# Kernel optimization log

Hardware: AMD Instinct MI355X
Metric: run time of the kernel (lower is better)

The kernel has to match this reference:

```python
import jax, jax.numpy as jnp
import numpy as np

EMBED_DIM = 768
NUM_HEADS = 12
HEAD_DIM = EMBED_DIM // NUM_HEADS
SCALE = HEAD_DIM ** -0.5


def setup_inputs() -> dict:
    key = jax.random.key(0)
    k_x, k_qkv, k_pw, k_pb = jax.random.split(key, 4)
    B, N = 2, 4096
    x = jax.random.normal(k_x, (B, N, EMBED_DIM), dtype=jnp.float32)
    # nn.Linear weights stored as [out, in]; we keep [in, out] for x @ W
    w_qkv = jax.random.normal(k_qkv, (EMBED_DIM, 3 * EMBED_DIM), dtype=jnp.float32) * (EMBED_DIM ** -0.5)
    w_proj = jax.random.normal(k_pw, (EMBED_DIM, EMBED_DIM), dtype=jnp.float32) * (EMBED_DIM ** -0.5)
    b_proj = jax.random.normal(k_pb, (EMBED_DIM,), dtype=jnp.float32) * 0.02
    return {"x": x, "w_qkv": w_qkv, "w_proj": w_proj, "b_proj": b_proj}


def reference(x, w_qkv, w_proj, b_proj):
    B, N, D = x.shape
    H, hd = NUM_HEADS, HEAD_DIM
    qkv = x @ w_qkv                                   # [B, N, 3*D]
    qkv = qkv.reshape(B, N, 3, H, hd)                 # matches '(qkv h d)' split order
    q, k, v = (qkv[:, :, i].transpose(0, 2, 1, 3) for i in range(3))  # each [B, H, N, hd]
    attn = jnp.einsum('bhid,bhjd->bhij', q, k) * SCALE  # [B, H, N, N] fully materialized
    attn = jax.nn.softmax(attn, axis=-1)
    out = jnp.einsum('bhij,bhjd->bhid', attn, v)        # [B, H, N, hd]
    out = out.transpose(0, 2, 1, 3).reshape(B, N, D)    # 'b h n d -> b n (h d)'
    return out @ w_proj + b_proj
```

## Files before the change

### kernel.cpp

```cpp
#include <hip/hip_runtime.h>
#include <hip/hip_bf16.h>

typedef __attribute__((ext_vector_type(4))) float f32x4;
typedef __attribute__((ext_vector_type(4))) int i32x4;
typedef __attribute__((ext_vector_type(8))) short s16x8;

static constexpr int NB = 2, NH = 12, SEQ = 4096, DM = 768, HD = 64;
static constexpr int ROWS = NB * SEQ;
static constexpr float QSC = 0.125f * 1.44269504f;

#define MFMA(a, b, c) __builtin_amdgcn_mfma_f32_16x16x32_bf16((a), (b), (c), 0, 0, 0)

typedef const void __attribute__((address_space(1)))* gas_t;
typedef void __attribute__((address_space(3)))* las_t;

__device__ __forceinline__ short f2bf(float f) {
  union { float f; unsigned u; } v; v.f = f;
  unsigned r = v.u + 0x7fffu + ((v.u >> 16) & 1u);
  return (short)(r >> 16);
}

__device__ __forceinline__ float exp2v(float x) {
  float r; asm("v_exp_f32 %0, %1" : "=v"(r) : "v"(x)); return r;
}

__global__ __launch_bounds__(256) void k_cast4(const float* __restrict__ in,
                                               short* __restrict__ out, int n4) {
  int i = blockIdx.x * 256 + threadIdx.x;
  if (i < n4) {
    float4 v = reinterpret_cast<const float4*>(in)[i];
    short4 o = { f2bf(v.x), f2bf(v.y), f2bf(v.z), f2bf(v.w) };
    reinterpret_cast<short4*>(out)[i] = o;
  }
}

__global__ __launch_bounds__(256) void k_tcast2(const float* __restrict__ in,
                                                short* __restrict__ out, int r, int c) {
  __shared__ short tile[32][33];
  int tpc = c >> 5;
  int by = blockIdx.x / tpc, bx = blockIdx.x % tpc;
  int tx = threadIdx.x & 31, ty = threadIdx.x >> 5;
#pragma unroll
  for (int i = 0; i < 4; ++i)
    tile[ty + i * 8][tx] = f2bf(in[(size_t)(by * 32 + ty + i * 8) * c + bx * 32 + tx]);
  __syncthreads();
#pragma unroll
  for (int i = 0; i < 4; ++i)
    out[(size_t)(bx * 32 + ty + i * 8) * r + by * 32 + tx] = tile[tx][ty + i * 8];
}

__device__ __forceinline__ void gemm128(const short* __restrict__ A,
                                        const short* __restrict__ Bt,
                                        int K, int row0, int col0,
                                        short As[2][4096], short Bs[2][4096],
                                        f32x4 acc[4][4]) {
  int w = threadIdx.x >> 6, l = threadIdx.x & 63;
  int q = l & 15, g = l >> 4;
  int wr = w >> 1, wc = w & 1;
  int sr = w * 16 + (l >> 2);
  int sc = (l & 3) * 8;

#define STG(buf, k0)                                                           \
  {                                                                            \
    _Pragma("unroll")                                                          \
    for (int i = 0; i < 2; ++i) {                                              \
      __builtin_amdgcn_global_load_lds(                                        \
          (gas_t)(A + (size_t)(row0 + i * 64 + sr) * K + (k0) + sc),           \
          (las_t)&As[buf][i * 2048 + w * 512], 16, 0, 0);                      \
      __builtin_amdgcn_global_load_lds(                                        \
          (gas_t)(Bt + (size_t)(col0 + i * 64 + sr) * K + (k0) + sc),          \
          (las_t)&Bs[buf][i * 2048 + w * 512], 16, 0, 0);                      \
    }                                                                          \
  }

  STG(0, 0);
  __syncthreads();
  int cur = 0;
  for (int k0 = 0; k0 < K; k0 += 32) {
    if (k0 + 32 < K) STG(cur ^ 1, k0 + 32);
    s16x8 af[4], bf[4];
#pragma unroll
    for (int m = 0; m < 4; ++m)
      af[m] = *reinterpret_cast<const s16x8*>(&As[cur][(wr * 64 + m * 16 + q) * 32 + g * 8]);
#pragma unroll
    for (int n = 0; n < 4; ++n)
      bf[n] = *reinterpret_cast<const s16x8*>(&Bs[cur][(wc * 64 + n * 16 + q) * 32 + g * 8]);
#pragma unroll
    for (int m = 0; m < 4; ++m)
#pragma unroll
      for (int n = 0; n < 4; ++n)
        acc[m][n] = MFMA(af[m], bf[n], acc[m][n]);
    __syncthreads();
    cur ^= 1;
  }
#undef STG
}

__global__ __launch_bounds__(256) void k_gemm_qkv2(const short* __restrict__ xb,
                                                   const short* __restrict__ wt,
                                                   short* __restrict__ qw,
                                                   short* __restrict__ kw,
                                                   short* __restrict__ vtw) {
  __shared__ __align__(16) short As[2][4096], Bs[2][4096];
  int bid = blockIdx.x;
  int swz = (bid & 7) * 144 + (bid >> 3);
  int brow = swz / 18, bcol = swz % 18;
  int row0 = brow * 128, col0 = bcol * 128;
  f32x4 acc[4][4] = {};
  gemm128(xb, wt, DM, row0, col0, As, Bs, acc);

  int w = threadIdx.x >> 6, l = threadIdx.x & 63;
  int q = l & 15, g = l >> 4;
  int wr = w >> 1, wc = w & 1;
  int cb = col0 + wc * 64;
  int which = cb / DM, h = (cb % DM) >> 6;
  int rowb = row0 + wr * 64;
  int b = rowb >> 12;
  int bh = b * NH + h;
#pragma unroll
  for (int m = 0; m < 4; ++m) {
#pragma unroll
    for (int n = 0; n < 4; ++n) {
      int d = n * 16 + q;
      if (which == 2) {
        int nseq = (rowb & 4095) + m * 16 + g * 4;
        short4 ov = { f2bf(acc[m][n][0]), f2bf(acc[m][n][1]),
                      f2bf(acc[m][n][2]), f2bf(acc[m][n][3]) };
        *reinterpret_cast<short4*>(&vtw[((size_t)bh * HD + d) * SEQ + nseq]) = ov;
      } else {
        short* dst = (which == 0) ? qw : kw;
        float sc = (which == 0) ? QSC : 1.f;
#pragma unroll
        for (int r = 0; r < 4; ++r) {
          int nseq = (rowb & 4095) + m * 16 + g * 4 + r;
          dst[((size_t)bh * SEQ + nseq) * HD + d] = f2bf(acc[m][n][r] * sc);
        }
      }
    }
  }
}

__global__ __launch_bounds__(256) void k_gemm_proj2(const short* __restrict__ aob,
                                                    const short* __restrict__ wt,
                                                    const float* __restrict__ bias,
                                                    float* __restrict__ out) {
  __shared__ __align__(16) short As[2][4096], Bs[2][4096];
  int bid = blockIdx.x;
  int swz = (bid & 7) * 48 + (bid >> 3);
  int brow = swz / 6, bcol = swz % 6;
  int row0 = brow * 128, col0 = bcol * 128;
  f32x4 acc[4][4] = {};
  gemm128(aob, wt, DM, row0, col0, As, Bs, acc);

  int w = threadIdx.x >> 6, l = threadIdx.x & 63;
  int q = l & 15, g = l >> 4;
  int wr = w >> 1, wc = w & 1;
#pragma unroll
  for (int m = 0; m < 4; ++m)
#pragma unroll
    for (int n = 0; n < 4; ++n) {
      int col = col0 + wc * 64 + n * 16 + q;
      float bv = bias[col];
#pragma unroll
      for (int r = 0; r < 4; ++r) {
        int row = row0 + wr * 64 + m * 16 + g * 4 + r;
        out[(size_t)row * DM + col] = acc[m][n][r] + bv;
      }
    }
}

__global__ __launch_bounds__(256, 2) void k_attn13(const short* __restrict__ qw,
                                                   const short* __restrict__ kw,
                                                   const short* __restrict__ vtw,
                                                   short* __restrict__ ao) {
  __shared__ __align__(16) short lds[2][2][4096];

  int bid = blockIdx.x;
  int swz = (bid & 7) * 48 + (bid >> 3);
  int bh = swz >> 4;
  int qchunk = swz & 15;

  int w = threadIdx.x >> 6, l = threadIdx.x & 63;
  int q = l & 15, g = l >> 4;

  const short* Kg = kw + (size_t)bh * SEQ * HD;
  const short* Vg = vtw + (size_t)bh * HD * SEQ;

  int ss = (l & 7) ^ (l >> 3) ^ ((w & 1) << 2);
  int rst = w * 8 + (l >> 3);

  int qbase = qchunk * 256 + w * 64;
  s16x8 qf[4][2];
#pragma unroll
  for (int qt = 0; qt < 4; ++qt)
#pragma unroll
    for (int kh = 0; kh < 2; ++kh)
      qf[qt][kh] = *reinterpret_cast<const s16x8*>(
          qw + ((size_t)bh * SEQ + qbase + qt * 16 + q) * HD + kh * 32 + g * 8);

  s16x8 ones;
  {
    short o1 = (q == 0) ? (short)0x3F80 : (short)0;
#pragma unroll
    for (int i = 0; i < 8; ++i) ones[i] = o1;
  }

  f32x4 o[4][4] = {};
  f32x4 lsa[4] = {};

#define STAGE(buf, t)                                                              \
  {                                                                                \
    int key0 = (t) * 64;                                                           \
    _Pragma("unroll")                                                              \
    for (int i = 0; i < 2; ++i) {                                                  \
      const short* gk = Kg + (size_t)(key0 + i * 32 + rst) * HD + ss * 8;          \
      __builtin_amdgcn_global_load_lds((gas_t)gk,                                  \
          (las_t)&lds[buf][0][i * 2048 + w * 512], 16, 0, 0);                      \
      const short* gv = Vg + (size_t)(i * 32 + rst) * SEQ + key0 + ss * 8;         \
      __builtin_amdgcn_global_load_lds((gas_t)gv,                                  \
          (las_t)&lds[buf][1][i * 2048 + w * 512], 16, 0, 0);                      \
    }                                                                              \
  }

#define TBODY(CUR, NXT, tt, DO_STAGE)                                              \
  {                                                                                \
    if (DO_STAGE) STAGE(NXT, (tt) + 1);                                            \
    f32x4 s[2][2][4] = {};                              \
    __builtin_amdgcn_s_setprio(1);                                                 \
    _Pragma("unroll")                                                              \
    for (int c = 0; c < 2; ++c)                                                    \
      _Pragma("unroll")                                                            \
      for (int ab = 0; ab < 2; ++ab) {                                             \
        int R = c * 32 + ab * 4 + ((q >> 2) << 3) + (q & 3);                       \
        int sw = (R & 7) ^ (((R >> 3) & 1) << 2);                                  \
        _Pragma("unroll")                                                          \
        for (int kh = 0; kh < 2; ++kh) {                                           \
          int slot = (kh * 4 + g) ^ sw;                                            \
          s16x8 af = *reinterpret_cast<const s16x8*>(                              \
              &lds[CUR][0][R * 64 + slot * 8]);                                    \
          _Pragma("unroll")                                                        \
          for (int qt = 0; qt < 4; ++qt)                                           \
            s[c][ab][qt] = MFMA(af, qf[qt][kh], s[c][ab][qt]);                     \
        }                                                                          \
      }                                                                            \
    __builtin_amdgcn_s_setprio(0);                                                 \
    i32x4 pv[2][4];                                    \
    _Pragma("unroll")                                                              \
    for (int qt = 0; qt < 4; ++qt) {                                               \
      unsigned u[16];                                                              \
      _Pragma("unroll")                                                            \
      for (int i = 0; i < 16; ++i)                                                 \
        u[i] = __float_as_uint(exp2v(s[i >> 3][(i >> 2) & 1][qt][i & 3]));         \
      _Pragma("unroll")                                                            \
      for (int c = 0; c < 2; ++c)                                                  \
        _Pragma("unroll")                                                          \
        for (int j = 0; j < 4; ++j)                                                \
          pv[c][qt][j] = (int)__builtin_amdgcn_perm(u[c * 8 + 2 * j + 1],          \
                                                    u[c * 8 + 2 * j],              \
                                                    0x07060302u);                  \
    }                                                                              \
    __builtin_amdgcn_s_setprio(1);                                                 \
    _Pragma("unroll")                                                              \
    for (int c = 0; c < 2; ++c) {                                                  \
      _Pragma("unroll")                                                            \
      for (int dt = 0; dt < 4; ++dt) {                                             \
        int R = dt * 16 + q;                                                       \
        int sw = (R & 7) ^ (((R >> 3) & 1) << 2);                                  \
        int slot = (c * 4 + g) ^ sw;                                               \
        s16x8 vf = *reinterpret_cast<const s16x8*>(                                \
            &lds[CUR][1][R * 64 + slot * 8]);                                      \
        _Pragma("unroll")                                                          \
        for (int qt = 0; qt < 4; ++qt)                                             \
          o[qt][dt] = MFMA(vf, __builtin_bit_cast(s16x8, pv[c][qt]), o[qt][dt]);   \
      }                                                                            \
      _Pragma("unroll")                                                            \
      for (int qt = 0; qt < 4; ++qt)                                               \
        lsa[qt] = MFMA(ones, __builtin_bit_cast(s16x8, pv[c][qt]), lsa[qt]);       \
    }                                                                              \
    __builtin_amdgcn_s_setprio(0);                                                 \
    __syncthreads();                                                               \
  }

  STAGE(0, 0);
  __syncthreads();

  for (int t = 0; t < SEQ / 64 - 2; t += 2) {
    TBODY(0, 1, t, true);
    TBODY(1, 0, t + 1, true);
  }
  TBODY(0, 1, SEQ / 64 - 2, true);
  TBODY(1, 0, SEQ / 64 - 1, false);
#undef TBODY
#undef STAGE

  int b = bh / NH, h = bh % NH;
#pragma unroll
  for (int qt = 0; qt < 4; ++qt) {
    float ls = __shfl(lsa[qt][0], q);
    float inv = 1.f / ls;
    size_t row = (size_t)b * SEQ + qbase + qt * 16 + q;
    short* op = ao + row * DM + h * HD;
#pragma unroll
    for (int dt = 0; dt < 4; ++dt) {
      short4 ov = { f2bf(o[qt][dt][0] * inv), f2bf(o[qt][dt][1] * inv),
                    f2bf(o[qt][dt][2] * inv), f2bf(o[qt][dt][3] * inv) };
      *reinterpret_cast<short4*>(op + dt * 16 + g * 4) = ov;
    }
  }
}

extern "C" void kernel_launch(void* const* d_in, const int* in_sizes, int n_in,
                              void* d_out, int out_size, void* d_ws, size_t ws_size,
                              hipStream_t stream) {
  const float* x      = (const float*)d_in[0];
  const float* w_qkv  = (const float*)d_in[1];
  const float* w_proj = (const float*)d_in[2];
  const float* b_proj = (const float*)d_in[3];
  float* out = (float*)d_out;

  char* p = (char*)d_ws;
  auto take = [&](size_t bytes) { char* r = p; p += (bytes + 255) & ~(size_t)255; return r; };
  short* xb     = (short*)take((size_t)ROWS * DM * 2);
  short* wtqkv  = (short*)take((size_t)3 * DM * DM * 2);
  short* wtproj = (short*)take((size_t)DM * DM * 2);
  short* qw     = (short*)take((size_t)NB * NH * SEQ * HD * 2);
  short* kw     = (short*)take((size_t)NB * NH * SEQ * HD * 2);
  short* vtw    = (short*)take((size_t)NB * NH * HD * SEQ * 2);
  short* ao     = (short*)take((size_t)ROWS * DM * 2);

  int n4 = ROWS * DM / 4;
  k_cast4<<<(n4 + 255) / 256, 256, 0, stream>>>(x, xb, n4);
  k_tcast2<<<(DM / 32) * (3 * DM / 32), 256, 0, stream>>>(w_qkv, wtqkv, DM, 3 * DM);
  k_tcast2<<<(DM / 32) * (DM / 32), 256, 0, stream>>>(w_proj, wtproj, DM, DM);
  k_gemm_qkv2<<<64 * 18, 256, 0, stream>>>(xb, wtqkv, qw, kw, vtw);
  k_attn13<<<NB * NH * (SEQ / 256), 256, 0, stream>>>(qw, kw, vtw, ao);
  k_gemm_proj2<<<64 * 6, 256, 0, stream>>>(ao, wtproj, b_proj, out);
}
```

Before: 192.4 us.

## Split attention over two key halves and merge partial outputs

Each attention block now handles only half of the key sequence, which doubles the grid from 384 to 768 blocks so work spreads more evenly across CUs. Each half writes unnormalized fp32 partial outputs and row sums to a workspace. A new merge kernel adds the two halves, normalizes, and writes the bf16 output. In exchange it adds extra fp32 global traffic and one more kernel launch.

```diff
diff --git a/kernel.cpp b/kernel.cpp
--- a/kernel.cpp
+++ b/kernel.cpp
@@ -7,6 +7,7 @@
 
 static constexpr int NB = 2, NH = 12, SEQ = 4096, DM = 768, HD = 64;
 static constexpr int ROWS = NB * SEQ;
+static constexpr int BHROWS = NB * NH * SEQ;
 static constexpr float QSC = 0.125f * 1.44269504f;
 
 #define MFMA(a, b, c) __builtin_amdgcn_mfma_f32_16x16x32_bf16((a), (b), (c), 0, 0, 0)
@@ -169,16 +170,19 @@
     }
 }
 
-__global__ __launch_bounds__(256, 2) void k_attn13(const short* __restrict__ qw,
+__global__ __launch_bounds__(256, 2) void k_attn14(const short* __restrict__ qw,
                                                    const short* __restrict__ kw,
                                                    const short* __restrict__ vtw,
-                                                   short* __restrict__ ao) {
+                                                   float* __restrict__ opart,
+                                                   float* __restrict__ lpart) {
   __shared__ __align__(16) short lds[2][2][4096];
 
   int bid = blockIdx.x;
-  int swz = (bid & 7) * 48 + (bid >> 3);
-  int bh = swz >> 4;
-  int qchunk = swz & 15;
+  int swz = (bid & 7) * 96 + (bid >> 3);
+  int bh = swz >> 5;
+  int rem = swz & 31;
+  int qchunk = rem >> 1;
+  int half = rem & 1;
 
   int w = threadIdx.x >> 6, l = threadIdx.x & 63;
   int q = l & 15, g = l >> 4;
@@ -188,6 +192,7 @@
 
   int ss = (l & 7) ^ (l >> 3) ^ ((w & 1) << 2);
   int rst = w * 8 + (l >> 3);
+  int kbase = half * (SEQ / 2);
 
   int qbase = qchunk * 256 + w * 64;
   s16x8 qf[4][2];
@@ -210,7 +215,7 @@
 
 #define STAGE(buf, t)                                                              \
   {                                                                                \
-    int key0 = (t) * 64;                                                           \
+    int key0 = kbase + (t) * 64;                                                   \
     _Pragma("unroll")                                                              \
     for (int i = 0; i < 2; ++i) {                                                  \
       const short* gk = Kg + (size_t)(key0 + i * 32 + rst) * HD + ss * 8;          \
@@ -284,29 +289,46 @@
   STAGE(0, 0);
   __syncthreads();
 
-  for (int t = 0; t < SEQ / 64 - 2; t += 2) {
+  for (int t = 0; t < SEQ / 128 - 2; t += 2) {
     TBODY(0, 1, t, true);
     TBODY(1, 0, t + 1, true);
   }
-  TBODY(0, 1, SEQ / 64 - 2, true);
-  TBODY(1, 0, SEQ / 64 - 1, false);
+  TBODY(0, 1, SEQ / 128 - 2, true);
+  TBODY(1, 0, SEQ / 128 - 1, false);
 #undef TBODY
 #undef STAGE
 
-  int b = bh / NH, h = bh % NH;
 #pragma unroll
   for (int qt = 0; qt < 4; ++qt) {
     float ls = __shfl(lsa[qt][0], q);
-    float inv = 1.f / ls;
-    size_t row = (size_t)b * SEQ + qbase + qt * 16 + q;
-    short* op = ao + row * DM + h * HD;
-#pragma unroll
-    for (int dt = 0; dt < 4; ++dt) {
-      short4 ov = { f2bf(o[qt][dt][0] * inv), f2bf(o[qt][dt][1] * inv),
-                    f2bf(o[qt][dt][2] * inv), f2bf(o[qt][dt][3] * inv) };
-      *reinterpret_cast<short4*>(op + dt * 16 + g * 4) = ov;
-    }
-  }
+    size_t prow = (size_t)bh * SEQ + qbase + qt * 16 + q;
+    float* op = opart + ((size_t)half * BHROWS + prow) * HD;
+#pragma unroll
+    for (int dt = 0; dt < 4; ++dt)
+      *reinterpret_cast<f32x4*>(op + dt * 16 + g * 4) = o[qt][dt];
+    if (g == 0)
+      lpart[(size_t)half * BHROWS + prow] = ls;
+  }
+}
+
+__global__ __launch_bounds__(256) void k_merge(const float* __restrict__ opart,
+                                               const float* __restrict__ lpart,
+                                               short* __restrict__ ao) {
+  int i = blockIdx.x * 256 + threadIdx.x;
+  if (i >= BHROWS * HD / 4) return;
+  int bhn = i >> 4;
+  int d4 = (i & 15) * 4;
+  const float* p0 = opart + (size_t)bhn * HD + d4;
+  const float* p1 = p0 + (size_t)BHROWS * HD;
+  f32x4 a = *reinterpret_cast<const f32x4*>(p0);
+  f32x4 b = *reinterpret_cast<const f32x4*>(p1);
+  float inv = 1.f / (lpart[bhn] + lpart[BHROWS + bhn]);
+  int bh = bhn >> 12, n = bhn & 4095;
+  int bb = bh / NH, h = bh % NH;
+  short* op = ao + ((size_t)(bb * SEQ + n)) * DM + h * HD + d4;
+  short4 ov = { f2bf((a[0] + b[0]) * inv), f2bf((a[1] + b[1]) * inv),
+                f2bf((a[2] + b[2]) * inv), f2bf((a[3] + b[3]) * inv) };
+  *reinterpret_cast<short4*>(op) = ov;
 }
 
 extern "C" void kernel_launch(void* const* d_in, const int* in_sizes, int n_in,
@@ -327,12 +349,15 @@
   short* kw     = (short*)take((size_t)NB * NH * SEQ * HD * 2);
   short* vtw    = (short*)take((size_t)NB * NH * HD * SEQ * 2);
   short* ao     = (short*)take((size_t)ROWS * DM * 2);
+  float* opart  = (float*)take((size_t)2 * BHROWS * HD * 4);
+  float* lpart  = (float*)take((size_t)2 * BHROWS * 4);
 
   int n4 = ROWS * DM / 4;
   k_cast4<<<(n4 + 255) / 256, 256, 0, stream>>>(x, xb, n4);
   k_tcast2<<<(DM / 32) * (3 * DM / 32), 256, 0, stream>>>(w_qkv, wtqkv, DM, 3 * DM);
   k_tcast2<<<(DM / 32) * (DM / 32), 256, 0, stream>>>(w_proj, wtproj, DM, DM);
   k_gemm_qkv2<<<64 * 18, 256, 0, stream>>>(xb, wtqkv, qw, kw, vtw);
-  k_attn13<<<NB * NH * (SEQ / 256), 256, 0, stream>>>(qw, kw, vtw, ao);
+  k_attn14<<<NB * NH * (SEQ / 256) * 2, 256, 0, stream>>>(qw, kw, vtw, opart, lpart);
+  k_merge<<<(BHROWS * HD / 4 + 255) / 256, 256, 0, stream>>>(opart, lpart, ao);
   k_gemm_proj2<<<64 * 6, 256, 0, stream>>>(ao, wtproj, b_proj, out);
 }
```

New measurement: 184.6 us. -4.1%, faster.
